# Kernel optimization log

Measured on AMD Instinct MI355X. Metric: run time of the kernel, lower is better.

The kernel has to match this reference:

```python
import jax, jax.numpy as jnp
import numpy as np

N_NODES = 100000
N_EDGES = 1_600_000
D = 32


def setup_inputs() -> dict:
    key = jax.random.key(0)
    k1, k2, k3, k4, k5 = jax.random.split(key, 5)
    x = jax.random.normal(k1, (N_NODES, D), dtype=jnp.float32)
    W1 = jax.random.normal(k2, (D, D), dtype=jnp.float32) * (1.0 / np.sqrt(D))
    W2 = jax.random.normal(k3, (D, D), dtype=jnp.float32) * (1.0 / np.sqrt(D))
    b2 = jax.random.normal(k4, (D,), dtype=jnp.float32) * 0.01
    edge_index = jax.random.randint(k5, (2, N_EDGES), 0, N_NODES, dtype=jnp.int64)
    return {"x": x, "W1": W1, "W2": W2, "b2": b2, "edge_index": edge_index}


def reference(x, W1, W2, b2, edge_index):
    # ptensors0.transfer0 over the graph: F1[i] = sum_{(j->i) in E} x[j]
    src = edge_index[0]
    dst = edge_index[1]
    F1 = jax.ops.segment_sum(x[src], dst, num_segments=x.shape[0])  # [N, D]
    # out = lin2(x) + lin1(F1)  (lin2 has bias, lin1 does not; torch Linear: y = x @ W.T + b)
    return x @ W2.T + b2 + F1 @ W1.T
```

## Files before the change

kernel.cpp:

```cpp
#include <hip/hip_runtime.h>
#include <hip/hip_bf16.h>

#define DIM 32
#define LOG_NPB 7
#define NPB 128
#define CAP 4096
#define NBINS 800
#define EPB 16384
#define EPT 16

__global__ __launch_bounds__(256) void fused_lin_kernel(
    const float* __restrict__ x,
    const float* __restrict__ W1,
    const float* __restrict__ W2,
    const float* __restrict__ b2,
    float* __restrict__ out,
    unsigned* __restrict__ y32,
    int* __restrict__ cursor, int nb,
    int n_nodes)
{
    __shared__ float xs[8][DIM];

    const int t = threadIdx.x;

    if (blockIdx.x == 0) {
        for (int i = t; i < nb; i += 256) cursor[i] = i * CAP;
    }

    const int r = t >> 5;
    const int c = t & 31;

    float4 w1r[8], w2r[8];
    #pragma unroll
    for (int q = 0; q < 8; ++q) {
        w1r[q] = *(const float4*)(W1 + c * DIM + q * 4);
        w2r[q] = *(const float4*)(W2 + c * DIM + q * 4);
    }
    const float bias = b2[c];

    const int ntiles = (n_nodes + 7) >> 3;

    for (int tile = blockIdx.x; tile < ntiles; tile += gridDim.x) {
        const int row = tile * 8 + r;
        __syncthreads();
        if (row < n_nodes) xs[r][c] = x[(long)row * DIM + c];
        __syncthreads();
        if (row < n_nodes) {
            const float4* xr = (const float4*)xs[r];
            float a2 = bias;
            float a1 = 0.0f;
            #pragma unroll
            for (int q = 0; q < 8; ++q) {
                float4 xv = xr[q];
                a2 += xv.x * w2r[q].x + xv.y * w2r[q].y + xv.z * w2r[q].z + xv.w * w2r[q].w;
                a1 += xv.x * w1r[q].x + xv.y * w1r[q].y + xv.z * w1r[q].z + xv.w * w1r[q].w;
            }
            out[(long)row * DIM + c] = a2;
            float hi = __shfl_down(a1, 1);
            if ((c & 1) == 0) {
                __hip_bfloat16 blo = __float2bfloat16(a1);
                __hip_bfloat16 bhi = __float2bfloat16(hi);
                unsigned pack = ((unsigned)(*(unsigned short*)&bhi) << 16)
                              | (unsigned)(*(unsigned short*)&blo);
                y32[(size_t)row * 16 + (c >> 1)] = pack;
            }
        }
    }
}

__global__ __launch_bounds__(1024) void bucket_scatter_kernel(
    const int* __restrict__ src, const int* __restrict__ dst,
    int* __restrict__ cursor, unsigned* __restrict__ bedges, int nE)
{
    __shared__ int cnt[NBINS];
    __shared__ int base[NBINS];

    const int t = threadIdx.x;
    const long blockStart = (long)blockIdx.x * EPB;

    for (int i = t; i < NBINS; i += 1024) cnt[i] = 0;
    __syncthreads();

    int es[EPT], ed[EPT], rk[EPT];
    #pragma unroll
    for (int i = 0; i < EPT; ++i) {
        long e = blockStart + (long)i * 1024 + t;
        if (e < nE) { es[i] = src[e]; ed[i] = dst[e]; }
        else        { es[i] = -1;     ed[i] = 0;      }
    }
    #pragma unroll
    for (int i = 0; i < EPT; ++i) {
        if (es[i] >= 0) rk[i] = atomicAdd(&cnt[ed[i] >> LOG_NPB], 1);
    }
    __syncthreads();

    for (int i = t; i < NBINS; i += 1024) {
        int c = cnt[i];
        if (c > 0) base[i] = atomicAdd(&cursor[i], c);
    }
    __syncthreads();

    #pragma unroll
    for (int i = 0; i < EPT; ++i) {
        if (es[i] >= 0) {
            int b = ed[i] >> LOG_NPB;
            int p = base[b] + rk[i];
            if (p < (b + 1) * CAP)
                bedges[p] = ((unsigned)es[i] << LOG_NPB) | (unsigned)(ed[i] & (NPB - 1));
        }
    }
}

__global__ __launch_bounds__(512) void sort_gather_kernel(
    const int* __restrict__ cursor, const unsigned* __restrict__ bedges,
    const unsigned short* __restrict__ yb,
    float* __restrict__ out, int n_nodes)
{
    __shared__ unsigned ent[CAP];
    __shared__ unsigned sorted[CAP];
    __shared__ int cnt[NPB];
    __shared__ int ex[NPB];
    __shared__ int cur[NPB];

    const int b = blockIdx.x;
    const int t = threadIdx.x;
    const int start = b * CAP;
    int n = cursor[b] - start;
    if (n > CAP) n = CAP;
    if (n < 0) n = 0;

    if (t < NPB) { cnt[t] = 0; cur[t] = 0; }
    __syncthreads();

    for (int i = t; i < n; i += 512) {
        unsigned e = bedges[start + i];
        ent[i] = e;
        atomicAdd(&cnt[e & (NPB - 1)], 1);
    }
    __syncthreads();

    if (t < NPB) ex[t] = cnt[t];
    __syncthreads();
    for (int off = 1; off < NPB; off <<= 1) {
        int add = 0;
        if (t < NPB && t >= off) add = ex[t - off];
        __syncthreads();
        if (t < NPB) ex[t] += add;
        __syncthreads();
    }
    if (t < NPB) ex[t] -= cnt[t];
    __syncthreads();

    for (int i = t; i < n; i += 512) {
        unsigned e = ent[i];
        int bin = (int)(e & (NPB - 1));
        int r = atomicAdd(&cur[bin], 1);
        sorted[ex[bin] + r] = e >> LOG_NPB;
    }
    __syncthreads();

    const int wv   = t >> 6;
    const int lane = t & 63;
    const int slot = lane >> 3;
    const int li   = lane & 7;

    int ln   = wv;
    int node = b * NPB + ln;
    if (node >= n_nodes) return;

    int st = ex[ln];
    int d  = cnt[ln];
    int s[4];
    #pragma unroll
    for (int k = 0; k < 4; ++k) {
        int e = slot + 8 * k;
        int idx = (e < d) ? e : (d > 0 ? d - 1 : 0);
        s[k] = (int)sorted[(d > 0 ? st : 0) + idx];
    }
    float4 o = make_float4(0.f, 0.f, 0.f, 0.f);
    if (slot == 0) o = ((const float4*)(out + ((size_t)node << 5)))[li];

    while (true) {
        ushort4 u[4];
        #pragma unroll
        for (int k = 0; k < 4; ++k) {
            if (8 * k < d)
                u[k] = *(const ushort4*)(yb + ((size_t)s[k] << 5) + (li << 2));
        }

        const int ln_n   = ln + 8;
        const int node_n = node + 8;
        const bool have_n = (ln_n < NPB) && (node_n < n_nodes);
        int st_n = 0, d_n = 0;
        int sn[4];
        float4 o_n = make_float4(0.f, 0.f, 0.f, 0.f);
        if (have_n) {
            st_n = ex[ln_n];
            d_n  = cnt[ln_n];
            #pragma unroll
            for (int k = 0; k < 4; ++k) {
                int e = slot + 8 * k;
                int idx = (e < d_n) ? e : (d_n > 0 ? d_n - 1 : 0);
                sn[k] = (int)sorted[(d_n > 0 ? st_n : 0) + idx];
            }
            if (slot == 0) o_n = ((const float4*)(out + ((size_t)node_n << 5)))[li];
        }

        float a0 = 0.f, a1 = 0.f, a2 = 0.f, a3 = 0.f;
        #pragma unroll
        for (int k = 0; k < 4; ++k) {
            if (8 * k < d) {
                const bool v = (slot + 8 * k) < d;
                a0 += v ? __uint_as_float((unsigned)u[k].x << 16) : 0.f;
                a1 += v ? __uint_as_float((unsigned)u[k].y << 16) : 0.f;
                a2 += v ? __uint_as_float((unsigned)u[k].z << 16) : 0.f;
                a3 += v ? __uint_as_float((unsigned)u[k].w << 16) : 0.f;
            }
        }
        for (int e0 = 32 + slot; e0 < d; e0 += 8) {
            int ss = (int)sorted[st + e0];
            ushort4 uu = *(const ushort4*)(yb + ((size_t)ss << 5) + (li << 2));
            a0 += __uint_as_float((unsigned)uu.x << 16);
            a1 += __uint_as_float((unsigned)uu.y << 16);
            a2 += __uint_as_float((unsigned)uu.z << 16);
            a3 += __uint_as_float((unsigned)uu.w << 16);
        }

        #pragma unroll
        for (int m = 8; m < 64; m <<= 1) {
            a0 += __shfl_xor(a0, m);
            a1 += __shfl_xor(a1, m);
            a2 += __shfl_xor(a2, m);
            a3 += __shfl_xor(a3, m);
        }

        if (slot == 0 && d > 0) {
            float4 w;
            w.x = o.x + a0; w.y = o.y + a1; w.z = o.z + a2; w.w = o.w + a3;
            ((float4*)(out + ((size_t)node << 5)))[li] = w;
        }

        if (!have_n) break;
        ln = ln_n; node = node_n; st = st_n; d = d_n;
        s[0] = sn[0]; s[1] = sn[1]; s[2] = sn[2]; s[3] = sn[3];
        o = o_n;
    }
}

extern "C" void kernel_launch(void* const* d_in, const int* in_sizes, int n_in,
                              void* d_out, int out_size, void* d_ws, size_t ws_size,
                              hipStream_t stream) {
    const float* x  = (const float*)d_in[0];
    const float* W1 = (const float*)d_in[1];
    const float* W2 = (const float*)d_in[2];
    const float* b2 = (const float*)d_in[3];
    const int*   ei = (const int*)d_in[4];

    const int n_nodes = in_sizes[0] / DIM;
    const int n_edges = in_sizes[4] / 2;
    const int* src = ei;
    const int* dst = ei + n_edges;
    float* out = (float*)d_out;

    const int nb = (n_nodes + NPB - 1) / NPB;

    char* basep = (char*)d_ws;
    size_t off = 0;
    auto alloc = [&](size_t bytes) {
        char* p = basep + off;
        off = (off + bytes + 255) & ~(size_t)255;
        return p;
    };
    unsigned* y32    = (unsigned*)alloc((size_t)n_nodes * DIM * sizeof(unsigned short));
    int*      cursor = (int*)     alloc((size_t)nb * sizeof(int));
    unsigned* bedges = (unsigned*)alloc((size_t)nb * CAP * sizeof(unsigned));
    (void)ws_size;

    fused_lin_kernel<<<1024, 256, 0, stream>>>(x, W1, W2, b2, out, y32, cursor, nb, n_nodes);
    bucket_scatter_kernel<<<(n_edges + EPB - 1) / EPB, 1024, 0, stream>>>(src, dst, cursor, bedges, n_edges);
    sort_gather_kernel<<<nb, 512, 0, stream>>>(cursor, bedges, (const unsigned short*)y32, out, n_nodes);
}
```

Before: 79.63 us.

## Fuse linear and bucket-scatter kernels into one launch, warp-shuffle prefix scan

Merges the dense linear kernel and the edge bucket-scatter kernel into a single heterogeneous launch, where the first blocks scatter edges and the remaining blocks compute the linear layers. Cursor initialisation moves to a memset, with cursors now relative per-bucket counts. The 128-bin exclusive scan in the sort kernel switches from a barrier-based shared-memory loop to a single-wavefront shuffle scan. The aim is to cut a launch boundary, let both stages run concurrently, and remove barriers; the cost is an added memset and larger blocks for the linear part.

```diff
diff --git a/kernel.cpp b/kernel.cpp
--- a/kernel.cpp
+++ b/kernel.cpp
@@ -8,105 +8,100 @@
 #define NBINS 800
 #define EPB 16384
 #define EPT 16
-
-__global__ __launch_bounds__(256) void fused_lin_kernel(
+#define LIN_BLOCKS 256
+
+__global__ __launch_bounds__(1024) void lin_scatter_kernel(
     const float* __restrict__ x,
     const float* __restrict__ W1,
     const float* __restrict__ W2,
     const float* __restrict__ b2,
     float* __restrict__ out,
     unsigned* __restrict__ y32,
-    int* __restrict__ cursor, int nb,
-    int n_nodes)
-{
-    __shared__ float xs[8][DIM];
-
-    const int t = threadIdx.x;
-
-    if (blockIdx.x == 0) {
-        for (int i = t; i < nb; i += 256) cursor[i] = i * CAP;
-    }
-
-    const int r = t >> 5;
-    const int c = t & 31;
-
-    float4 w1r[8], w2r[8];
-    #pragma unroll
-    for (int q = 0; q < 8; ++q) {
-        w1r[q] = *(const float4*)(W1 + c * DIM + q * 4);
-        w2r[q] = *(const float4*)(W2 + c * DIM + q * 4);
-    }
-    const float bias = b2[c];
-
-    const int ntiles = (n_nodes + 7) >> 3;
-
-    for (int tile = blockIdx.x; tile < ntiles; tile += gridDim.x) {
-        const int row = tile * 8 + r;
-        __syncthreads();
-        if (row < n_nodes) xs[r][c] = x[(long)row * DIM + c];
-        __syncthreads();
-        if (row < n_nodes) {
-            const float4* xr = (const float4*)xs[r];
-            float a2 = bias;
-            float a1 = 0.0f;
-            #pragma unroll
-            for (int q = 0; q < 8; ++q) {
-                float4 xv = xr[q];
-                a2 += xv.x * w2r[q].x + xv.y * w2r[q].y + xv.z * w2r[q].z + xv.w * w2r[q].w;
-                a1 += xv.x * w1r[q].x + xv.y * w1r[q].y + xv.z * w1r[q].z + xv.w * w1r[q].w;
-            }
-            out[(long)row * DIM + c] = a2;
-            float hi = __shfl_down(a1, 1);
-            if ((c & 1) == 0) {
-                __hip_bfloat16 blo = __float2bfloat16(a1);
-                __hip_bfloat16 bhi = __float2bfloat16(hi);
-                unsigned pack = ((unsigned)(*(unsigned short*)&bhi) << 16)
-                              | (unsigned)(*(unsigned short*)&blo);
-                y32[(size_t)row * 16 + (c >> 1)] = pack;
-            }
-        }
-    }
-}
-
-__global__ __launch_bounds__(1024) void bucket_scatter_kernel(
     const int* __restrict__ src, const int* __restrict__ dst,
-    int* __restrict__ cursor, unsigned* __restrict__ bedges, int nE)
+    int* __restrict__ cursor, unsigned* __restrict__ bedges,
+    int nE, int n_nodes, int nScat)
 {
     __shared__ int cnt[NBINS];
     __shared__ int base[NBINS];
+    __shared__ float xs[32][DIM];
 
     const int t = threadIdx.x;
-    const long blockStart = (long)blockIdx.x * EPB;
-
-    for (int i = t; i < NBINS; i += 1024) cnt[i] = 0;
-    __syncthreads();
-
-    int es[EPT], ed[EPT], rk[EPT];
-    #pragma unroll
-    for (int i = 0; i < EPT; ++i) {
-        long e = blockStart + (long)i * 1024 + t;
-        if (e < nE) { es[i] = src[e]; ed[i] = dst[e]; }
-        else        { es[i] = -1;     ed[i] = 0;      }
-    }
-    #pragma unroll
-    for (int i = 0; i < EPT; ++i) {
-        if (es[i] >= 0) rk[i] = atomicAdd(&cnt[ed[i] >> LOG_NPB], 1);
-    }
-    __syncthreads();
-
-    for (int i = t; i < NBINS; i += 1024) {
-        int c = cnt[i];
-        if (c > 0) base[i] = atomicAdd(&cursor[i], c);
-    }
-    __syncthreads();
-
-    #pragma unroll
-    for (int i = 0; i < EPT; ++i) {
-        if (es[i] >= 0) {
-            int b = ed[i] >> LOG_NPB;
-            int p = base[b] + rk[i];
-            if (p < (b + 1) * CAP)
-                bedges[p] = ((unsigned)es[i] << LOG_NPB) | (unsigned)(ed[i] & (NPB - 1));
+
+    if (blockIdx.x < nScat) {
+        const long blockStart = (long)blockIdx.x * EPB;
+
+        for (int i = t; i < NBINS; i += 1024) cnt[i] = 0;
+        __syncthreads();
+
+        int es[EPT], ed[EPT], rk[EPT];
+        #pragma unroll
+        for (int i = 0; i < EPT; ++i) {
+            long e = blockStart + (long)i * 1024 + t;
+            if (e < nE) { es[i] = src[e]; ed[i] = dst[e]; }
+            else        { es[i] = -1;     ed[i] = 0;      }
+        }
+        #pragma unroll
+        for (int i = 0; i < EPT; ++i) {
+            if (es[i] >= 0) rk[i] = atomicAdd(&cnt[ed[i] >> LOG_NPB], 1);
+        }
+        __syncthreads();
+
+        for (int i = t; i < NBINS; i += 1024) {
+            int c = cnt[i];
+            if (c > 0) base[i] = atomicAdd(&cursor[i], c);
+        }
+        __syncthreads();
+
+        #pragma unroll
+        for (int i = 0; i < EPT; ++i) {
+            if (es[i] >= 0) {
+                int b = ed[i] >> LOG_NPB;
+                int p = base[b] + rk[i];
+                if (p < CAP)
+                    bedges[b * CAP + p] =
+                        ((unsigned)es[i] << LOG_NPB) | (unsigned)(ed[i] & (NPB - 1));
+            }
+        }
+    } else {
+        const int lb = blockIdx.x - nScat;
+        const int r = t >> 5;
+        const int c = t & 31;
+
+        float4 w1r[8], w2r[8];
+        #pragma unroll
+        for (int q = 0; q < 8; ++q) {
+            w1r[q] = *(const float4*)(W1 + c * DIM + q * 4);
+            w2r[q] = *(const float4*)(W2 + c * DIM + q * 4);
+        }
+        const float bias = b2[c];
+
+        const int ntiles = (n_nodes + 31) >> 5;
+
+        for (int tile = lb; tile < ntiles; tile += LIN_BLOCKS) {
+            const int row = tile * 32 + r;
+            __syncthreads();
+            if (row < n_nodes) xs[r][c] = x[(long)row * DIM + c];
+            __syncthreads();
+            if (row < n_nodes) {
+                const float4* xr = (const float4*)xs[r];
+                float a2 = bias;
+                float a1 = 0.0f;
+                #pragma unroll
+                for (int q = 0; q < 8; ++q) {
+                    float4 xv = xr[q];
+                    a2 += xv.x * w2r[q].x + xv.y * w2r[q].y + xv.z * w2r[q].z + xv.w * w2r[q].w;
+                    a1 += xv.x * w1r[q].x + xv.y * w1r[q].y + xv.z * w1r[q].z + xv.w * w1r[q].w;
+                }
+                out[(long)row * DIM + c] = a2;
+                float hi = __shfl_down(a1, 1);
+                if ((c & 1) == 0) {
+                    __hip_bfloat16 blo = __float2bfloat16(a1);
+                    __hip_bfloat16 bhi = __float2bfloat16(hi);
+                    unsigned pack = ((unsigned)(*(unsigned short*)&bhi) << 16)
+                                  | (unsigned)(*(unsigned short*)&blo);
+                    y32[(size_t)row * 16 + (c >> 1)] = pack;
+                }
+            }
         }
     }
 }
@@ -125,7 +120,7 @@
     const int b = blockIdx.x;
     const int t = threadIdx.x;
     const int start = b * CAP;
-    int n = cursor[b] - start;
+    int n = cursor[b];
     if (n > CAP) n = CAP;
     if (n < 0) n = 0;
 
@@ -139,16 +134,19 @@
     }
     __syncthreads();
 
-    if (t < NPB) ex[t] = cnt[t];
-    __syncthreads();
-    for (int off = 1; off < NPB; off <<= 1) {
-        int add = 0;
-        if (t < NPB && t >= off) add = ex[t - off];
-        __syncthreads();
-        if (t < NPB) ex[t] += add;
-        __syncthreads();
-    }
-    if (t < NPB) ex[t] -= cnt[t];
+    if (t < 64) {
+        int c0 = cnt[2 * t];
+        int c1 = cnt[2 * t + 1];
+        int v  = c0 + c1;
+        #pragma unroll
+        for (int off = 1; off < 64; off <<= 1) {
+            int u = __shfl_up(v, off);
+            if (t >= off) v += u;
+        }
+        int pbase = v - (c0 + c1);
+        ex[2 * t]     = pbase;
+        ex[2 * t + 1] = pbase + c0;
+    }
     __syncthreads();
 
     for (int i = t; i < n; i += 512) {
@@ -276,7 +274,12 @@
     unsigned* bedges = (unsigned*)alloc((size_t)nb * CAP * sizeof(unsigned));
     (void)ws_size;
 
-    fused_lin_kernel<<<1024, 256, 0, stream>>>(x, W1, W2, b2, out, y32, cursor, nb, n_nodes);
-    bucket_scatter_kernel<<<(n_edges + EPB - 1) / EPB, 1024, 0, stream>>>(src, dst, cursor, bedges, n_edges);
-    sort_gather_kernel<<<nb, 512, 0, stream>>>(cursor, bedges, (const unsigned short*)y32, out, n_nodes);
+    hipMemsetAsync(cursor, 0, (size_t)nb * sizeof(int), stream);
+
+    const int nScat = (n_edges + EPB - 1) / EPB;
+    lin_scatter_kernel<<<nScat + LIN_BLOCKS, 1024, 0, stream>>>(
+        x, W1, W2, b2, out, y32, src, dst, cursor, bedges, n_edges, n_nodes, nScat);
+
+    sort_gather_kernel<<<nb, 512, 0, stream>>>(cursor, bedges,
+                                               (const unsigned short*)y32, out, n_nodes);
 }
```

New measurement: 83.33 us. +4.6%, slower.

## Sort edges per block locally and hand bins to gather via segment descriptors

Applied to the files above, without the earlier changes.

The scatter kernel now counting-sorts each block's edges by destination bin in shared memory and writes them back contiguously. Previously every edge was scattered into a global per-bin slot. Each bin's run is recorded as segment descriptors appended through a per-bin atomic counter. The gather kernel collects its bin's segments with 16-lane groups instead of reading one contiguous capped region. The aim is coalesced global writes in the scatter phase, at the cost of a descriptor indirection, smaller and less coalesced gather reads, and an extra memset launch.

```diff
diff --git a/kernel.cpp b/kernel.cpp
--- a/kernel.cpp
+++ b/kernel.cpp
@@ -4,10 +4,12 @@
 #define DIM 32
 #define LOG_NPB 7
 #define NPB 128
-#define CAP 4096
 #define NBINS 800
-#define EPB 16384
-#define EPT 16
+#define NBINS_PAD 1024
+#define EPB 6144
+#define EPT 12
+#define MAXSEG 384
+#define ENTCAP 4096
 
 __global__ __launch_bounds__(256) void fused_lin_kernel(
     const float* __restrict__ x,
@@ -16,17 +18,11 @@
     const float* __restrict__ b2,
     float* __restrict__ out,
     unsigned* __restrict__ y32,
-    int* __restrict__ cursor, int nb,
     int n_nodes)
 {
     __shared__ float xs[8][DIM];
 
     const int t = threadIdx.x;
-
-    if (blockIdx.x == 0) {
-        for (int i = t; i < nb; i += 256) cursor[i] = i * CAP;
-    }
-
     const int r = t >> 5;
     const int c = t & 31;
 
@@ -68,87 +64,143 @@
     }
 }
 
-__global__ __launch_bounds__(1024) void bucket_scatter_kernel(
+__global__ __launch_bounds__(512) void scatter_private_kernel(
     const int* __restrict__ src, const int* __restrict__ dst,
-    int* __restrict__ cursor, unsigned* __restrict__ bedges, int nE)
+    unsigned* __restrict__ blkedges, unsigned* __restrict__ desc,
+    int* __restrict__ nseg, int nE)
 {
-    __shared__ int cnt[NBINS];
-    __shared__ int base[NBINS];
+    __shared__ unsigned stage[EPB];
+    __shared__ int cnt[NBINS_PAD];
+    __shared__ int ex[NBINS_PAD];
+    __shared__ int wsum[8];
 
     const int t = threadIdx.x;
-    const long blockStart = (long)blockIdx.x * EPB;
-
-    for (int i = t; i < NBINS; i += 1024) cnt[i] = 0;
-    __syncthreads();
-
-    int es[EPT], ed[EPT], rk[EPT];
+    const long base = (long)blockIdx.x * EPB;
+
+    for (int i = t; i < NBINS_PAD; i += 512) cnt[i] = 0;
+    __syncthreads();
+
+    int bn[EPT], rk[EPT];
+    unsigned pk[EPT];
     #pragma unroll
     for (int i = 0; i < EPT; ++i) {
-        long e = blockStart + (long)i * 1024 + t;
-        if (e < nE) { es[i] = src[e]; ed[i] = dst[e]; }
-        else        { es[i] = -1;     ed[i] = 0;      }
-    }
+        long e = base + (long)i * 512 + t;
+        if (e < nE) {
+            int s  = src[e];
+            int dd = dst[e];
+            bn[i] = dd >> LOG_NPB;
+            pk[i] = ((unsigned)s << LOG_NPB) | (unsigned)(dd & (NPB - 1));
+            rk[i] = atomicAdd(&cnt[bn[i]], 1);
+        } else bn[i] = -1;
+    }
+    __syncthreads();
+
+    {
+        int c0 = cnt[2 * t];
+        int c1 = cnt[2 * t + 1];
+        int v  = c0 + c1;
+        const int lane = t & 63, wv = t >> 6;
+        #pragma unroll
+        for (int off = 1; off < 64; off <<= 1) {
+            int u = __shfl_up(v, off);
+            if (lane >= off) v += u;
+        }
+        if (lane == 63) wsum[wv] = v;
+        __syncthreads();
+        int woff = 0;
+        for (int w = 0; w < wv; ++w) woff += wsum[w];
+        int pbase = woff + v - (c0 + c1);
+        ex[2 * t]     = pbase;
+        ex[2 * t + 1] = pbase + c0;
+    }
+    __syncthreads();
+
     #pragma unroll
-    for (int i = 0; i < EPT; ++i) {
-        if (es[i] >= 0) rk[i] = atomicAdd(&cnt[ed[i] >> LOG_NPB], 1);
-    }
-    __syncthreads();
-
-    for (int i = t; i < NBINS; i += 1024) {
-        int c = cnt[i];
-        if (c > 0) base[i] = atomicAdd(&cursor[i], c);
-    }
-    __syncthreads();
-
-    #pragma unroll
-    for (int i = 0; i < EPT; ++i) {
-        if (es[i] >= 0) {
-            int b = ed[i] >> LOG_NPB;
-            int p = base[b] + rk[i];
-            if (p < (b + 1) * CAP)
-                bedges[p] = ((unsigned)es[i] << LOG_NPB) | (unsigned)(ed[i] & (NPB - 1));
+    for (int i = 0; i < EPT; ++i)
+        if (bn[i] >= 0) stage[ex[bn[i]] + rk[i]] = pk[i];
+    __syncthreads();
+
+    const int n_this = (int)((nE - base < (long)EPB) ? (nE - base) : EPB);
+    for (int i = t; i < n_this; i += 512)
+        blkedges[base + i] = stage[i];
+
+    for (int b = t; b < NBINS; b += 512) {
+        int c = cnt[b];
+        int gs = (int)base + ex[b];
+        while (c > 0) {
+            int cc = (c > 255) ? 255 : c;
+            int k = atomicAdd(&nseg[b], 1);
+            if (k < MAXSEG) desc[b * MAXSEG + k] = ((unsigned)gs << 8) | (unsigned)cc;
+            gs += cc; c -= cc;
         }
     }
 }
 
 __global__ __launch_bounds__(512) void sort_gather_kernel(
-    const int* __restrict__ cursor, const unsigned* __restrict__ bedges,
+    const int* __restrict__ nseg, const unsigned* __restrict__ desc,
+    const unsigned* __restrict__ blkedges,
     const unsigned short* __restrict__ yb,
     float* __restrict__ out, int n_nodes)
 {
-    __shared__ unsigned ent[CAP];
-    __shared__ unsigned sorted[CAP];
+    __shared__ unsigned ent[ENTCAP];
+    __shared__ unsigned sorted[ENTCAP];
     __shared__ int cnt[NPB];
     __shared__ int ex[NPB];
     __shared__ int cur[NPB];
+    __shared__ int segoff[MAXSEG];
+    __shared__ int tot;
 
     const int b = blockIdx.x;
     const int t = threadIdx.x;
-    const int start = b * CAP;
-    int n = cursor[b] - start;
-    if (n > CAP) n = CAP;
-    if (n < 0) n = 0;
-
+
+    if (t == 0) tot = 0;
     if (t < NPB) { cnt[t] = 0; cur[t] = 0; }
     __syncthreads();
 
-    for (int i = t; i < n; i += 512) {
-        unsigned e = bedges[start + i];
-        ent[i] = e;
-        atomicAdd(&cnt[e & (NPB - 1)], 1);
-    }
-    __syncthreads();
-
-    if (t < NPB) ex[t] = cnt[t];
-    __syncthreads();
-    for (int off = 1; off < NPB; off <<= 1) {
-        int add = 0;
-        if (t < NPB && t >= off) add = ex[t - off];
-        __syncthreads();
-        if (t < NPB) ex[t] += add;
-        __syncthreads();
-    }
-    if (t < NPB) ex[t] -= cnt[t];
+    int ns = nseg[b];
+    if (ns > MAXSEG) ns = MAXSEG;
+
+    for (int si = t; si < ns; si += 512) {
+        int c = (int)(desc[b * MAXSEG + si] & 255u);
+        segoff[si] = atomicAdd(&tot, c);
+    }
+    __syncthreads();
+    int n = tot;
+    if (n > ENTCAP) n = ENTCAP;
+
+    {
+        const int g   = t >> 4;
+        const int l16 = t & 15;
+        for (int si = g; si < ns; si += 32) {
+            unsigned dc = desc[b * MAXSEG + si];
+            int c  = (int)(dc & 255u);
+            int gs = (int)(dc >> 8);
+            int o  = segoff[si];
+            for (int j = l16; j < c; j += 16) {
+                int oo = o + j;
+                if (oo < ENTCAP) {
+                    unsigned e = blkedges[gs + j];
+                    ent[oo] = e;
+                    atomicAdd(&cnt[e & (NPB - 1)], 1);
+                }
+            }
+        }
+    }
+    __syncthreads();
+
+    if (t < 64) {
+        int c0 = cnt[2 * t];
+        int c1 = cnt[2 * t + 1];
+        int v  = c0 + c1;
+        #pragma unroll
+        for (int off = 1; off < 64; off <<= 1) {
+            int u = __shfl_up(v, off);
+            if (t >= off) v += u;
+        }
+        int pbase = v - (c0 + c1);
+        ex[2 * t]     = pbase;
+        ex[2 * t + 1] = pbase + c0;
+    }
     __syncthreads();
 
     for (int i = t; i < n; i += 512) {
@@ -271,12 +323,17 @@
         off = (off + bytes + 255) & ~(size_t)255;
         return p;
     };
-    unsigned* y32    = (unsigned*)alloc((size_t)n_nodes * DIM * sizeof(unsigned short));
-    int*      cursor = (int*)     alloc((size_t)nb * sizeof(int));
-    unsigned* bedges = (unsigned*)alloc((size_t)nb * CAP * sizeof(unsigned));
+    unsigned* y32      = (unsigned*)alloc((size_t)n_nodes * DIM * sizeof(unsigned short));
+    unsigned* blkedges = (unsigned*)alloc((size_t)n_edges * sizeof(unsigned));
+    unsigned* desc     = (unsigned*)alloc((size_t)nb * MAXSEG * sizeof(unsigned));
+    int*      nseg     = (int*)     alloc((size_t)nb * sizeof(int));
     (void)ws_size;
 
-    fused_lin_kernel<<<1024, 256, 0, stream>>>(x, W1, W2, b2, out, y32, cursor, nb, n_nodes);
-    bucket_scatter_kernel<<<(n_edges + EPB - 1) / EPB, 1024, 0, stream>>>(src, dst, cursor, bedges, n_edges);
-    sort_gather_kernel<<<nb, 512, 0, stream>>>(cursor, bedges, (const unsigned short*)y32, out, n_nodes);
+    hipMemsetAsync(nseg, 0, (size_t)nb * sizeof(int), stream);
+
+    fused_lin_kernel<<<1024, 256, 0, stream>>>(x, W1, W2, b2, out, y32, n_nodes);
+    scatter_private_kernel<<<(n_edges + EPB - 1) / EPB, 512, 0, stream>>>(
+        src, dst, blkedges, desc, nseg, n_edges);
+    sort_gather_kernel<<<nb, 512, 0, stream>>>(nseg, desc, blkedges,
+                                               (const unsigned short*)y32, out, n_nodes);
 }
```

Result: slower. 93.08 us (+16.9%).

## Move x@W2+b2 into gather kernel and use wave-shuffle prefix scan

Applied to the files above, without the earlier changes.

The W2 linear plus bias is no longer computed in the first kernel, which wrote it to out. It is now computed in the gather kernel, where each 8-lane slot group multiplies its 4-element slice of x by a register-held W2 tile. Partial products are folded into the same shuffle reduction used for the neighbour sum. This removes one full write and re-read of the output tensor. The shared-memory Hillis-Steele scan over 128 bins, with a barrier per step, is replaced by a single-wave shuffle scan. The cost is more registers and extra FMA work in the gather kernel.

```diff
diff --git a/kernel.cpp b/kernel.cpp
--- a/kernel.cpp
+++ b/kernel.cpp
@@ -9,12 +9,9 @@
 #define EPB 16384
 #define EPT 16
 
-__global__ __launch_bounds__(256) void fused_lin_kernel(
+__global__ __launch_bounds__(256) void lin_y_kernel(
     const float* __restrict__ x,
     const float* __restrict__ W1,
-    const float* __restrict__ W2,
-    const float* __restrict__ b2,
-    float* __restrict__ out,
     unsigned* __restrict__ y32,
     int* __restrict__ cursor, int nb,
     int n_nodes)
@@ -22,7 +19,6 @@
     __shared__ float xs[8][DIM];
 
     const int t = threadIdx.x;
-
     if (blockIdx.x == 0) {
         for (int i = t; i < nb; i += 256) cursor[i] = i * CAP;
     }
@@ -30,13 +26,10 @@
     const int r = t >> 5;
     const int c = t & 31;
 
-    float4 w1r[8], w2r[8];
-    #pragma unroll
-    for (int q = 0; q < 8; ++q) {
+    float4 w1r[8];
+    #pragma unroll
+    for (int q = 0; q < 8; ++q)
         w1r[q] = *(const float4*)(W1 + c * DIM + q * 4);
-        w2r[q] = *(const float4*)(W2 + c * DIM + q * 4);
-    }
-    const float bias = b2[c];
 
     const int ntiles = (n_nodes + 7) >> 3;
 
@@ -47,15 +40,12 @@
         __syncthreads();
         if (row < n_nodes) {
             const float4* xr = (const float4*)xs[r];
-            float a2 = bias;
             float a1 = 0.0f;
             #pragma unroll
             for (int q = 0; q < 8; ++q) {
                 float4 xv = xr[q];
-                a2 += xv.x * w2r[q].x + xv.y * w2r[q].y + xv.z * w2r[q].z + xv.w * w2r[q].w;
                 a1 += xv.x * w1r[q].x + xv.y * w1r[q].y + xv.z * w1r[q].z + xv.w * w1r[q].w;
             }
-            out[(long)row * DIM + c] = a2;
             float hi = __shfl_down(a1, 1);
             if ((c & 1) == 0) {
                 __hip_bfloat16 blo = __float2bfloat16(a1);
@@ -114,6 +104,9 @@
 __global__ __launch_bounds__(512) void sort_gather_kernel(
     const int* __restrict__ cursor, const unsigned* __restrict__ bedges,
     const unsigned short* __restrict__ yb,
+    const float* __restrict__ x,
+    const float* __restrict__ W2,
+    const float* __restrict__ b2,
     float* __restrict__ out, int n_nodes)
 {
     __shared__ unsigned ent[CAP];
@@ -124,6 +117,19 @@
 
     const int b = blockIdx.x;
     const int t = threadIdx.x;
+    const int wv   = t >> 6;
+    const int lane = t & 63;
+    const int slot = lane >> 3;
+    const int li   = lane & 7;
+
+    float w2t[4][4];
+    #pragma unroll
+    for (int j = 0; j < 4; ++j)
+        #pragma unroll
+        for (int k = 0; k < 4; ++k)
+            w2t[k][j] = W2[(size_t)(4 * li + j) * DIM + 4 * slot + k];
+    const float4 bias = ((const float4*)b2)[li];
+
     const int start = b * CAP;
     int n = cursor[b] - start;
     if (n > CAP) n = CAP;
@@ -139,16 +145,19 @@
     }
     __syncthreads();
 
-    if (t < NPB) ex[t] = cnt[t];
-    __syncthreads();
-    for (int off = 1; off < NPB; off <<= 1) {
-        int add = 0;
-        if (t < NPB && t >= off) add = ex[t - off];
-        __syncthreads();
-        if (t < NPB) ex[t] += add;
-        __syncthreads();
-    }
-    if (t < NPB) ex[t] -= cnt[t];
+    if (t < 64) {
+        int c0 = cnt[2 * t];
+        int c1 = cnt[2 * t + 1];
+        int v  = c0 + c1;
+        #pragma unroll
+        for (int off = 1; off < 64; off <<= 1) {
+            int u = __shfl_up(v, off);
+            if (t >= off) v += u;
+        }
+        int pbase = v - (c0 + c1);
+        ex[2 * t]     = pbase;
+        ex[2 * t + 1] = pbase + c0;
+    }
     __syncthreads();
 
     for (int i = t; i < n; i += 512) {
@@ -159,11 +168,6 @@
     }
     __syncthreads();
 
-    const int wv   = t >> 6;
-    const int lane = t & 63;
-    const int slot = lane >> 3;
-    const int li   = lane & 7;
-
     int ln   = wv;
     int node = b * NPB + ln;
     if (node >= n_nodes) return;
@@ -177,8 +181,7 @@
         int idx = (e < d) ? e : (d > 0 ? d - 1 : 0);
         s[k] = (int)sorted[(d > 0 ? st : 0) + idx];
     }
-    float4 o = make_float4(0.f, 0.f, 0.f, 0.f);
-    if (slot == 0) o = ((const float4*)(out + ((size_t)node << 5)))[li];
+    float4 xv = ((const float4*)(x + ((size_t)node << 5)))[slot];
 
     while (true) {
         ushort4 u[4];
@@ -193,7 +196,7 @@
         const bool have_n = (ln_n < NPB) && (node_n < n_nodes);
         int st_n = 0, d_n = 0;
         int sn[4];
-        float4 o_n = make_float4(0.f, 0.f, 0.f, 0.f);
+        float4 xv_n = make_float4(0.f, 0.f, 0.f, 0.f);
         if (have_n) {
             st_n = ex[ln_n];
             d_n  = cnt[ln_n];
@@ -203,10 +206,15 @@
                 int idx = (e < d_n) ? e : (d_n > 0 ? d_n - 1 : 0);
                 sn[k] = (int)sorted[(d_n > 0 ? st_n : 0) + idx];
             }
-            if (slot == 0) o_n = ((const float4*)(out + ((size_t)node_n << 5)))[li];
-        }
-
-        float a0 = 0.f, a1 = 0.f, a2 = 0.f, a3 = 0.f;
+            xv_n = ((const float4*)(x + ((size_t)node_n << 5)))[slot];
+        }
+
+        float a0, a1, a2, a3;
+        a0 = xv.x * w2t[0][0] + xv.y * w2t[1][0] + xv.z * w2t[2][0] + xv.w * w2t[3][0];
+        a1 = xv.x * w2t[0][1] + xv.y * w2t[1][1] + xv.z * w2t[2][1] + xv.w * w2t[3][1];
+        a2 = xv.x * w2t[0][2] + xv.y * w2t[1][2] + xv.z * w2t[2][2] + xv.w * w2t[3][2];
+        a3 = xv.x * w2t[0][3] + xv.y * w2t[1][3] + xv.z * w2t[2][3] + xv.w * w2t[3][3];
+
         #pragma unroll
         for (int k = 0; k < 4; ++k) {
             if (8 * k < d) {
@@ -234,16 +242,19 @@
             a3 += __shfl_xor(a3, m);
         }
 
-        if (slot == 0 && d > 0) {
+        if (slot == 0) {
             float4 w;
-            w.x = o.x + a0; w.y = o.y + a1; w.z = o.z + a2; w.w = o.w + a3;
+            w.x = a0 + bias.x;
+            w.y = a1 + bias.y;
+            w.z = a2 + bias.z;
+            w.w = a3 + bias.w;
             ((float4*)(out + ((size_t)node << 5)))[li] = w;
         }
 
         if (!have_n) break;
         ln = ln_n; node = node_n; st = st_n; d = d_n;
         s[0] = sn[0]; s[1] = sn[1]; s[2] = sn[2]; s[3] = sn[3];
-        o = o_n;
+        xv = xv_n;
     }
 }
 
@@ -276,7 +287,8 @@
     unsigned* bedges = (unsigned*)alloc((size_t)nb * CAP * sizeof(unsigned));
     (void)ws_size;
 
-    fused_lin_kernel<<<1024, 256, 0, stream>>>(x, W1, W2, b2, out, y32, cursor, nb, n_nodes);
+    lin_y_kernel<<<1024, 256, 0, stream>>>(x, W1, y32, cursor, nb, n_nodes);
     bucket_scatter_kernel<<<(n_edges + EPB - 1) / EPB, 1024, 0, stream>>>(src, dst, cursor, bedges, n_edges);
-    sort_gather_kernel<<<nb, 512, 0, stream>>>(cursor, bedges, (const unsigned short*)y32, out, n_nodes);
-}
+    sort_gather_kernel<<<nb, 512, 0, stream>>>(cursor, bedges, (const unsigned short*)y32,
+                                               x, W2, b2, out, n_nodes);
+}
```

After: 78.20 us. No clear change (-1.8%).
